# Kernel tuning notes

Hardware: AMD Instinct MI355X
Metric: run time of the kernel (lower is better)

## Reference

```python
import jax, jax.numpy as jnp
import numpy as np

FACTOR = 2  # StyleGAN upsample factor
K1D = jnp.array([1.0, 4.0, 6.0, 4.0, 1.0], dtype=jnp.float32)
# StyleGAN upfirdn padding for upsample: p = kw - factor = 3
# pad0 = (p+1)//2 + factor - 1 = 3 ; pad1 = p//2 = 1 (+1 extra trailing zero
# because lhs_dilation gives length 2D-1 while zero-insertion gives 2D)
PAD0, PAD1 = 3, 2


def _upfir_axis(x, k1d, axis):
    """Zero-insert (factor 2) + 5-tap FIR along one spatial axis, depthwise.

    x: [N, C, D, H, W]; axis in {2, 3, 4}.
    """
    C = x.shape[1]
    kshape = [1, 1, 1]
    kshape[axis - 2] = k1d.shape[0]
    kernel = jnp.broadcast_to(k1d.reshape(kshape), (C, 1) + tuple(kshape))
    dil = [1, 1, 1]
    dil[axis - 2] = FACTOR
    pad = [(0, 0)] * 3
    pad[axis - 2] = (PAD0, PAD1)
    return jax.lax.conv_general_dilated(
        x, kernel.astype(x.dtype),
        window_strides=(1, 1, 1), padding=pad, lhs_dilation=dil,
        dimension_numbers=('NCDHW', 'OIDHW', 'NCDHW'),
        feature_group_count=C)


def setup_inputs() -> dict:
    key = jax.random.key(0)
    x = jax.random.normal(key, (4, 32, 48, 48, 48), dtype=jnp.float32)
    return {"x": x}


def reference(x):
    # normalize so kernel sums to 1, then apply gain factor per axis so the
    # total gain is factor**3 (StyleGAN: k = k/sum(k) * gain * factor**ndim,
    # split evenly across the 3 separable passes -> factor per axis)
    k = (K1D / K1D.sum() * FACTOR).astype(x.dtype)
    for ax in (2, 3, 4):  # D, H, W
        x = _upfir_axis(x, k, ax)
    return x  # [N, C, 2D, 2H, 2W]
```

## Files before the change

kernel.cpp:

```cpp
#include <hip/hip_runtime.h>


#define IN_D 48
#define IN_H 48
#define IN_W 48
#define NC   128
#define TD   6
#define TH   16
#define NTX  24
#define NTHREADS (NTX * TH)
#define LZ (TD + 2)
#define LY (TH + 2)
#define LX (IN_W + 2)
#define LXP (LX + 1)
#define NROWS (LZ * LY)

__device__ __forceinline__ float4 f4_even(float4 a, float4 b) {
    return make_float4(0.5f * (a.x + b.x), 0.5f * (a.y + b.y),
                       0.5f * (a.z + b.z), 0.5f * (a.w + b.w));
}
__device__ __forceinline__ float4 f4_odd(float4 a, float4 b, float4 c) {
    return make_float4(0.125f * (a.x + c.x) + 0.75f * b.x,
                       0.125f * (a.y + c.y) + 0.75f * b.y,
                       0.125f * (a.z + c.z) + 0.75f * b.z,
                       0.125f * (a.w + c.w) + 0.75f * b.w);
}

struct Q { float4 E, O; };

__global__ __launch_bounds__(NTHREADS)
void upfir3d_kernel(const float* __restrict__ in,
                    float* __restrict__ out) {
    __shared__ float lds[NROWS * LXP];

    const int tx = threadIdx.x;
    const int ty = threadIdx.y;
    const int bh = blockIdx.x;
    const int dz = blockIdx.y;
    const int nc = blockIdx.z;

    const int ih0 = bh * TH;
    const int id0 = dz * TD;
    const size_t in_base = (size_t)nc * (IN_D * IN_H * IN_W);

    const int tid = ty * NTX + tx;

    if (tid < 2 * NROWS) {
        int row = tid >> 1;
        int col = (tid & 1) ? (LX - 1) : 0;
        lds[row * LXP + col] = 0.0f;
    }

    {
        const int q = tid % 12;
        const int r = tid / 12;
        for (int row = r; row < NROWS; row += NTHREADS / 12) {
            int z  = row / LY;
            int y  = row - z * LY;
            int gd = id0 - 1 + z;
            int gh = ih0 - 1 + y;
            float4 v = make_float4(0.f, 0.f, 0.f, 0.f);
            if ((unsigned)gd < (unsigned)IN_D && (unsigned)gh < (unsigned)IN_H) {
                v = *reinterpret_cast<const float4*>(
                        in + in_base + ((size_t)gd * IN_H + gh) * IN_W + 4 * q);
            }
            float* dst = &lds[row * LXP + 1 + 4 * q];
            dst[0] = v.x; dst[1] = v.y; dst[2] = v.z; dst[3] = v.w;
        }
    }
    __syncthreads();

    const int ly = ty + 1;
    const int c0 = 2 * tx;

    auto whpart = [&](int z) -> Q {
        const float* p = &lds[(z * LY + (ly - 1)) * LXP + c0];
        float4 r[3];
#pragma unroll
        for (int dy = 0; dy < 3; ++dy) {
            float v0 = p[dy * LXP + 0];
            float v1 = p[dy * LXP + 1];
            float v2 = p[dy * LXP + 2];
            float v3 = p[dy * LXP + 3];
            r[dy].x = 0.5f * (v0 + v1);
            r[dy].y = 0.125f * (v0 + v2) + 0.75f * v1;
            r[dy].z = 0.5f * (v1 + v2);
            r[dy].w = 0.125f * (v1 + v3) + 0.75f * v2;
        }
        Q q;
        q.E = f4_even(r[0], r[1]);
        q.O = f4_odd(r[0], r[1], r[2]);
        return q;
    };

    Q qm = whpart(0);
    Q qc = whpart(1);

    const int OD = 2 * IN_D, OH = 2 * IN_H, OW = 2 * IN_W;
    const int ow = 4 * tx;
    const int oh = 2 * (ih0 + ty);
    float* ob = out + (size_t)nc * OD * OH * OW;

#pragma unroll
    for (int d = 0; d < TD; ++d) {
        Q qp = whpart(d + 2);
        const int od = 2 * (id0 + d);

        size_t b0 = ((size_t)od * OH + oh) * OW + ow;
        *reinterpret_cast<float4*>(ob + b0)      = f4_even(qm.E, qc.E);
        *reinterpret_cast<float4*>(ob + b0 + OW) = f4_even(qm.O, qc.O);

        size_t b1 = b0 + (size_t)OH * OW;
        *reinterpret_cast<float4*>(ob + b1)      = f4_odd(qm.E, qc.E, qp.E);
        *reinterpret_cast<float4*>(ob + b1 + OW) = f4_odd(qm.O, qc.O, qp.O);

        qm = qc;
        qc = qp;
    }
}

extern "C" void kernel_launch(void* const* d_in, const int* in_sizes, int n_in,
                              void* d_out, int out_size, void* d_ws, size_t ws_size,
                              hipStream_t stream) {
    const float* x = (const float*)d_in[0];
    float* out = (float*)d_out;

    dim3 grid(IN_H / TH, IN_D / TD, NC);
    dim3 block(NTX, TH, 1);
    upfir3d_kernel<<<grid, block, 0, stream>>>(x, out);
}
```

Before: 483.8 us.

## Assign one output row per thread with parity-selected H weights and float2 LDS reads

The thread-to-output mapping changes so each thread produces one output H row instead of an even/odd pair, with the row parity choosing the H-filter weights at runtime. The tile changes to 8 D slices by 8 input H rows, and the LDS row pitch becomes 52 so rows can be read as float2. This halves per-thread register state and the stores issued per loop iteration, and it doubles the blocks along H. The cost is that the W-direction work is repeated, since both threads of a row pair recompute it from the same LDS rows.

```diff
diff --git a/kernel.cpp b/kernel.cpp
--- a/kernel.cpp
+++ b/kernel.cpp
@@ -5,14 +5,14 @@
 #define IN_H 48
 #define IN_W 48
 #define NC   128
-#define TD   6
-#define TH   16
+#define TD   8
+#define THI  8
 #define NTX  24
-#define NTHREADS (NTX * TH)
+#define NTY  16
+#define NTHREADS (NTX * NTY)
 #define LZ (TD + 2)
-#define LY (TH + 2)
-#define LX (IN_W + 2)
-#define LXP (LX + 1)
+#define LY (THI + 2)
+#define LXP 52
 #define NROWS (LZ * LY)
 
 __device__ __forceinline__ float4 f4_even(float4 a, float4 b) {
@@ -26,8 +26,6 @@
                        0.125f * (a.w + c.w) + 0.75f * b.w);
 }
 
-struct Q { float4 E, O; };
-
 __global__ __launch_bounds__(NTHREADS)
 void upfir3d_kernel(const float* __restrict__ in,
                     float* __restrict__ out) {
@@ -39,22 +37,21 @@
     const int dz = blockIdx.y;
     const int nc = blockIdx.z;
 
-    const int ih0 = bh * TH;
+    const int ih0 = bh * THI;
     const int id0 = dz * TD;
-    const size_t in_base = (size_t)nc * (IN_D * IN_H * IN_W);
+    const float* inb = in + (size_t)nc * (IN_D * IN_H * IN_W);
 
     const int tid = ty * NTX + tx;
 
     if (tid < 2 * NROWS) {
         int row = tid >> 1;
-        int col = (tid & 1) ? (LX - 1) : 0;
+        int col = (tid & 1) ? 49 : 0;
         lds[row * LXP + col] = 0.0f;
     }
 
     {
         const int q = tid % 12;
-        const int r = tid / 12;
-        for (int row = r; row < NROWS; row += NTHREADS / 12) {
+        for (int row = tid / 12; row < NROWS; row += NTHREADS / 12) {
             int z  = row / LY;
             int y  = row - z * LY;
             int gd = id0 - 1 + z;
@@ -62,7 +59,7 @@
             float4 v = make_float4(0.f, 0.f, 0.f, 0.f);
             if ((unsigned)gd < (unsigned)IN_D && (unsigned)gh < (unsigned)IN_H) {
                 v = *reinterpret_cast<const float4*>(
-                        in + in_base + ((size_t)gd * IN_H + gh) * IN_W + 4 * q);
+                        inb + ((size_t)gd * IN_H + gh) * IN_W + 4 * q);
             }
             float* dst = &lds[row * LXP + 1 + 4 * q];
             dst[0] = v.x; dst[1] = v.y; dst[2] = v.z; dst[3] = v.w;
@@ -70,49 +67,47 @@
     }
     __syncthreads();
 
-    const int ly = ty + 1;
-    const int c0 = 2 * tx;
+    const int p   = ty & 1;
+    const float wga = p ? 0.125f : 0.5f;
+    const float wgb = p ? 0.75f  : 0.5f;
+    const float wgc = p ? 0.125f : 0.0f;
+    const int yy0 = ty >> 1;
+    const int cx  = 2 * tx;
 
-    auto whpart = [&](int z) -> Q {
-        const float* p = &lds[(z * LY + (ly - 1)) * LXP + c0];
-        float4 r[3];
+    auto whpart = [&](int z) -> float4 {
+        const float* pp = &lds[(z * LY + yy0) * LXP + cx];
+        float4 q4 = make_float4(0.f, 0.f, 0.f, 0.f);
 #pragma unroll
         for (int dy = 0; dy < 3; ++dy) {
-            float v0 = p[dy * LXP + 0];
-            float v1 = p[dy * LXP + 1];
-            float v2 = p[dy * LXP + 2];
-            float v3 = p[dy * LXP + 3];
-            r[dy].x = 0.5f * (v0 + v1);
-            r[dy].y = 0.125f * (v0 + v2) + 0.75f * v1;
-            r[dy].z = 0.5f * (v1 + v2);
-            r[dy].w = 0.125f * (v1 + v3) + 0.75f * v2;
+            const float wt = (dy == 0) ? wga : (dy == 1) ? wgb : wgc;
+            float2 a = *reinterpret_cast<const float2*>(pp + dy * LXP);
+            float2 b = *reinterpret_cast<const float2*>(pp + dy * LXP + 2);
+            float w0 = 0.5f   * (a.x + a.y);
+            float w1 = 0.125f * (a.x + b.x) + 0.75f * a.y;
+            float w2 = 0.5f   * (a.y + b.x);
+            float w3 = 0.125f * (a.y + b.y) + 0.75f * b.x;
+            q4.x += wt * w0; q4.y += wt * w1;
+            q4.z += wt * w2; q4.w += wt * w3;
         }
-        Q q;
-        q.E = f4_even(r[0], r[1]);
-        q.O = f4_odd(r[0], r[1], r[2]);
-        return q;
+        return q4;
     };
 
-    Q qm = whpart(0);
-    Q qc = whpart(1);
+    float4 qm = whpart(0);
+    float4 qc = whpart(1);
 
-    const int OD = 2 * IN_D, OH = 2 * IN_H, OW = 2 * IN_W;
-    const int ow = 4 * tx;
-    const int oh = 2 * (ih0 + ty);
-    float* ob = out + (size_t)nc * OD * OH * OW;
+    const int OH = 2 * IN_H, OW = 2 * IN_W;
+    const int orow = 2 * ih0 + ty;
+    float* ob = out + (size_t)nc * (2 * IN_D * OH * OW)
+                    + (size_t)orow * OW + 4 * tx;
+    const size_t plane = (size_t)OH * OW;
 
 #pragma unroll
     for (int d = 0; d < TD; ++d) {
-        Q qp = whpart(d + 2);
+        float4 qp = whpart(d + 2);
         const int od = 2 * (id0 + d);
 
-        size_t b0 = ((size_t)od * OH + oh) * OW + ow;
-        *reinterpret_cast<float4*>(ob + b0)      = f4_even(qm.E, qc.E);
-        *reinterpret_cast<float4*>(ob + b0 + OW) = f4_even(qm.O, qc.O);
-
-        size_t b1 = b0 + (size_t)OH * OW;
-        *reinterpret_cast<float4*>(ob + b1)      = f4_odd(qm.E, qc.E, qp.E);
-        *reinterpret_cast<float4*>(ob + b1 + OW) = f4_odd(qm.O, qc.O, qp.O);
+        *reinterpret_cast<float4*>(ob + (size_t)od * plane)       = f4_even(qm, qc);
+        *reinterpret_cast<float4*>(ob + (size_t)(od + 1) * plane) = f4_odd(qm, qc, qp);
 
         qm = qc;
         qc = qp;
@@ -125,7 +120,7 @@
     const float* x = (const float*)d_in[0];
     float* out = (float*)d_out;
 
-    dim3 grid(IN_H / TH, IN_D / TD, NC);
-    dim3 block(NTX, TH, 1);
+    dim3 grid(IN_H / THI, IN_D / TD, NC);
+    dim3 block(NTX, NTY, 1);
     upfir3d_kernel<<<grid, block, 0, stream>>>(x, out);
 }
```

After: 480.5 us. No clear change (-0.7%).
